# Performance work log

Measured on AMD Instinct MI355X. Metric: run time of the kernel, lower is better.

## Reference

```python
import jax, jax.numpy as jnp
import numpy as np

N_HEADS = 16
D_MODEL = 1024
D_HEAD = 64
B, T = 2, 2048


def setup_inputs() -> dict:
    key = jax.random.key(0)
    k1, k2, k3, k4 = jax.random.split(key, 4)
    query = jax.random.normal(k1, (B, T, D_MODEL), dtype=jnp.float32)
    query_mask = jnp.ones((B, T), dtype=bool)
    attn_prior = jax.random.uniform(k2, (B, T, T), dtype=jnp.float32)
    Wqkv = jax.random.normal(k3, (D_MODEL, 3 * N_HEADS * D_HEAD), dtype=jnp.float32) * (D_MODEL ** -0.5)
    Wo = jax.random.normal(k4, (N_HEADS * D_HEAD, D_MODEL), dtype=jnp.float32) * ((N_HEADS * D_HEAD) ** -0.5)
    return {"query": query, "query_mask": query_mask, "attn_prior": attn_prior, "Wqkv": Wqkv, "Wo": Wo}


def reference(query, query_mask, attn_prior, Wqkv, Wo):
    Bq, Tq, C = query.shape
    H, dh = N_HEADS, D_HEAD
    scale = dh ** -0.5
    qkv = query @ Wqkv  # (B, T, 3*H*dh)
    q, k, v = jnp.split(qkv, 3, axis=-1)
    q = q.reshape(Bq, Tq, H, dh).transpose(0, 2, 1, 3)  # (B, H, T, dh)
    k = k.reshape(Bq, Tq, H, dh).transpose(0, 2, 1, 3)
    v = v.reshape(Bq, Tq, H, dh).transpose(0, 2, 1, 3)

    attn_score = jnp.einsum('bhqd,bhkd->bhqk', q, k) * scale  # (B, H, T, T)

    # padding mask (B,1,T,1)*(B,1,1,T) -> (B,1,T,T)
    pad_mask = query_mask[:, None, :, None] & query_mask[:, None, None, :]
    neg_inf = jnp.float32(-jnp.inf)
    attn_score = jnp.where(pad_mask, attn_score, neg_inf)
    # causal mask
    causal = jnp.tril(jnp.ones((Tq, Tq), dtype=bool))
    attn_score = jnp.where(causal[None, None], attn_score, neg_inf)

    # training-mode log-domain prior mixing (make_prior_window_strict=False)
    eps = jnp.finfo(jnp.float32).tiny
    prior = attn_prior[:, :Tq][:, None] + eps  # (B, 1, T, T)
    attn_score_log = jax.nn.log_softmax(attn_score, axis=-1) + jnp.log(prior)
    attn_prob = jax.nn.softmax(attn_score_log, axis=-1)

    attn_prob = jnp.where(pad_mask, attn_prob, 0.0)
    y = jnp.einsum('bhqk,bhkd->bhqd', attn_prob, v)  # (B, H, T, dh)
    y = y.transpose(0, 2, 1, 3).reshape(Bq, Tq, H * dh)
    out = y @ Wo  # (B, T, d_model)
    return out, attn_prob, attn_score
```

## Files before the change

kernel.cpp:

```cpp
#include <hip/hip_runtime.h>
#include <math.h>

#define T_SEQ 2048
#define NHEADS 16
#define DHEAD 64
#define NB 2
#define DMODEL 1024
#define EPS_TINY 1.17549435e-38f
#define NEG_BIG -3.0e38f

__global__ __launch_bounds__(256) void sgemm_kernel(
    const float* __restrict__ A, const float* __restrict__ B,
    float* __restrict__ C, int M, int N, int K)
{
    __shared__ float As[8][128];
    __shared__ float Bs[8][132];
    const int tid = threadIdx.x;
    const int ty = tid >> 4, tx = tid & 15;
    const int m0 = blockIdx.y * 128, n0 = blockIdx.x * 128;

    const int ar = tid >> 1, ac = (tid & 1) << 2;
    const int br = tid >> 5, bc = (tid & 31) << 2;
    const float* Ap = A + (size_t)(m0 + ar) * K + ac;
    const float* Bp = B + (size_t)br * N + n0 + bc;

    float acc[8][8];
    #pragma unroll
    for (int i = 0; i < 8; ++i)
        #pragma unroll
        for (int j = 0; j < 8; ++j) acc[i][j] = 0.f;

    float4 av = *(const float4*)(Ap);
    float4 bv = *(const float4*)(Bp);

    for (int k0 = 0; k0 < K; k0 += 8) {
        __syncthreads();
        As[ac+0][ar] = av.x; As[ac+1][ar] = av.y;
        As[ac+2][ar] = av.z; As[ac+3][ar] = av.w;
        *(float4*)&Bs[br][bc] = bv;
        __syncthreads();
        if (k0 + 8 < K) {
            av = *(const float4*)(Ap + k0 + 8);
            bv = *(const float4*)(Bp + (size_t)(k0 + 8) * N);
        }
        #pragma unroll
        for (int kk = 0; kk < 8; ++kk) {
            float4 a0 = *(const float4*)&As[kk][ty*8];
            float4 a1 = *(const float4*)&As[kk][ty*8+4];
            float4 b0 = *(const float4*)&Bs[kk][tx*8];
            float4 b1 = *(const float4*)&Bs[kk][tx*8+4];
            float a[8] = {a0.x,a0.y,a0.z,a0.w,a1.x,a1.y,a1.z,a1.w};
            float bb[8] = {b0.x,b0.y,b0.z,b0.w,b1.x,b1.y,b1.z,b1.w};
            #pragma unroll
            for (int i = 0; i < 8; ++i)
                #pragma unroll
                for (int j = 0; j < 8; ++j)
                    acc[i][j] = fmaf(a[i], bb[j], acc[i][j]);
        }
    }
    #pragma unroll
    for (int i = 0; i < 8; ++i) {
        float* crow = C + (size_t)(m0 + ty*8 + i) * N + n0 + tx*8;
        *(float4*)crow     = make_float4(acc[i][0],acc[i][1],acc[i][2],acc[i][3]);
        *(float4*)(crow+4) = make_float4(acc[i][4],acc[i][5],acc[i][6],acc[i][7]);
    }
}

#define SW(r, g) ((((g) ^ ((r) >> 2)) & 15) << 2)

__global__ __launch_bounds__(256) void attn_chunk_kernel(
    const float* __restrict__ qkv, const float* __restrict__ prior,
    float* __restrict__ score, float* __restrict__ party, float* __restrict__ partml)
{
    __shared__ float Qs[64][64];
    __shared__ float KVs[64][64];
    __shared__ float Ps[64][64];

    const int tid = threadIdx.x;
    const int ty = tid >> 4, tx = tid & 15;

    const int f = 79 - (int)blockIdx.x;
    int qt, c;
    if (f < 8)       { qt = f;                      c = 0; }
    else if (f < 24) { qt = 8 + ((f - 8) >> 1);     c = (f - 8) & 1; }
    else if (f < 48) { int g = f - 24; int q3 = g / 3; qt = 16 + q3; c = g - q3*3; }
    else             { int g = f - 48; qt = 24 + (g >> 2); c = g & 3; }
    const int kt0 = c << 3;
    const int kt1 = min(kt0 + 7, qt);

    const int bh = blockIdx.y;
    const int b = bh >> 4, h = bh & 15;
    const int i0 = qt << 6;
    const float scale = 0.125f;

    const float* qbase = qkv + (size_t)b * T_SEQ * (3*DMODEL) + h * DHEAD;
    const float* kbase = qbase + DMODEL;
    float* srow = score + ((size_t)bh * T_SEQ + i0) * T_SEQ;

    #pragma unroll
    for (int u = 0; u < 4; ++u) {
        int idx = tid + (u << 8);
        int r = idx >> 4, g = idx & 15;
        float4 qv = *(const float4*)(qbase + (size_t)(i0 + r) * (3*DMODEL) + (g << 2));
        *(float4*)&Qs[r][SW(r, g)] = qv;
    }

    float m_i[4], l_i[4], y[4][4];
    #pragma unroll
    for (int i = 0; i < 4; ++i) {
        m_i[i] = -INFINITY; l_i[i] = 0.f;
        #pragma unroll
        for (int j = 0; j < 4; ++j) y[i][j] = 0.f;
    }

    for (int kt = kt0; kt <= kt1; ++kt) {
        const int c0 = kt << 6;
        float4 vpre[4];
        __syncthreads();
        #pragma unroll
        for (int u = 0; u < 4; ++u) {
            int idx = tid + (u << 8);
            int r = idx >> 4, g = idx & 15;
            const float* kp = kbase + (size_t)(c0 + r) * (3*DMODEL) + (g << 2);
            float4 kv = *(const float4*)kp;
            vpre[u] = *(const float4*)(kp + DMODEL);
            *(float4*)&KVs[r][SW(r, g)] = kv;
        }
        __syncthreads();

        float acc[4][4];
        #pragma unroll
        for (int i = 0; i < 4; ++i)
            #pragma unroll
            for (int j = 0; j < 4; ++j) acc[i][j] = 0.f;
        #pragma unroll 8
        for (int d4 = 0; d4 < 16; ++d4) {
            float4 a[4], bb[4];
            #pragma unroll
            for (int i = 0; i < 4; ++i)
                a[i] = *(const float4*)&Qs[(ty<<2)+i][SW((ty<<2)+i, d4)];
            #pragma unroll
            for (int j = 0; j < 4; ++j)
                bb[j] = *(const float4*)&KVs[(tx<<2)+j][SW((tx<<2)+j, d4)];
            #pragma unroll
            for (int i = 0; i < 4; ++i)
                #pragma unroll
                for (int j = 0; j < 4; ++j) {
                    acc[i][j] = fmaf(a[i].x, bb[j].x, acc[i][j]);
                    acc[i][j] = fmaf(a[i].y, bb[j].y, acc[i][j]);
                    acc[i][j] = fmaf(a[i].z, bb[j].z, acc[i][j]);
                    acc[i][j] = fmaf(a[i].w, bb[j].w, acc[i][j]);
                }
        }

        #pragma unroll
        for (int i = 0; i < 4; ++i) {
            const int rloc = (ty<<2) + i;
            const int row = i0 + rloc;
            const int cb = c0 + (tx<<2);
            float4 pv = *(const float4*)(prior + ((size_t)b*T_SEQ + row)*T_SEQ + cb);
            float s0 = (cb+0 <= row) ? acc[i][0]*scale : NEG_BIG;
            float s1 = (cb+1 <= row) ? acc[i][1]*scale : NEG_BIG;
            float s2 = (cb+2 <= row) ? acc[i][2]*scale : NEG_BIG;
            float s3 = (cb+3 <= row) ? acc[i][3]*scale : NEG_BIG;
            *(float4*)(srow + (size_t)rloc*T_SEQ + cb) = make_float4(s0,s1,s2,s3);
            float t0 = s0 + logf(pv.x + EPS_TINY);
            float t1 = s1 + logf(pv.y + EPS_TINY);
            float t2 = s2 + logf(pv.z + EPS_TINY);
            float t3 = s3 + logf(pv.w + EPS_TINY);
            float mt = fmaxf(fmaxf(t0,t1), fmaxf(t2,t3));
            #pragma unroll
            for (int off = 1; off < 16; off <<= 1)
                mt = fmaxf(mt, __shfl_xor(mt, off, 64));
            float mn = fmaxf(m_i[i], mt);
            float alpha = expf(m_i[i] - mn);
            float p0 = expf(t0 - mn), p1 = expf(t1 - mn),
                  p2 = expf(t2 - mn), p3 = expf(t3 - mn);
            float ps = p0 + p1 + p2 + p3;
            #pragma unroll
            for (int off = 1; off < 16; off <<= 1)
                ps += __shfl_xor(ps, off, 64);
            l_i[i] = l_i[i]*alpha + ps;
            m_i[i] = mn;
            y[i][0]*=alpha; y[i][1]*=alpha; y[i][2]*=alpha; y[i][3]*=alpha;
            *(float4*)&Ps[rloc][SW(rloc, tx)] = make_float4(p0,p1,p2,p3);
        }
        __syncthreads();
        #pragma unroll
        for (int u = 0; u < 4; ++u) {
            int idx = tid + (u << 8);
            int r = idx >> 4, g = idx & 15;
            *(float4*)&KVs[r][SW(r, g)] = vpre[u];
        }
        __syncthreads();

        #pragma unroll 8
        for (int J = 0; J < 16; ++J) {
            float4 p[4], vv[4];
            #pragma unroll
            for (int i = 0; i < 4; ++i)
                p[i] = *(const float4*)&Ps[(ty<<2)+i][SW((ty<<2)+i, J)];
            #pragma unroll
            for (int m = 0; m < 4; ++m)
                vv[m] = *(const float4*)&KVs[(J<<2)+m][SW((J<<2)+m, tx)];
            #pragma unroll
            for (int i = 0; i < 4; ++i) {
                y[i][0] = fmaf(p[i].x, vv[0].x, y[i][0]);
                y[i][0] = fmaf(p[i].y, vv[1].x, y[i][0]);
                y[i][0] = fmaf(p[i].z, vv[2].x, y[i][0]);
                y[i][0] = fmaf(p[i].w, vv[3].x, y[i][0]);
                y[i][1] = fmaf(p[i].x, vv[0].y, y[i][1]);
                y[i][1] = fmaf(p[i].y, vv[1].y, y[i][1]);
                y[i][1] = fmaf(p[i].z, vv[2].y, y[i][1]);
                y[i][1] = fmaf(p[i].w, vv[3].y, y[i][1]);
                y[i][2] = fmaf(p[i].x, vv[0].z, y[i][2]);
                y[i][2] = fmaf(p[i].y, vv[1].z, y[i][2]);
                y[i][2] = fmaf(p[i].z, vv[2].z, y[i][2]);
                y[i][2] = fmaf(p[i].w, vv[3].z, y[i][2]);
                y[i][3] = fmaf(p[i].x, vv[0].w, y[i][3]);
                y[i][3] = fmaf(p[i].y, vv[1].w, y[i][3]);
                y[i][3] = fmaf(p[i].z, vv[2].w, y[i][3]);
                y[i][3] = fmaf(p[i].w, vv[3].w, y[i][3]);
            }
        }
    }

    float* yp  = party  + ((((size_t)bh*32 + qt)*4 + c) << 12);
    float* mlp = partml + ((((size_t)bh*32 + qt)*4 + c) << 7);
    #pragma unroll
    for (int i = 0; i < 4; ++i) {
        const int rloc = (ty<<2) + i;
        *(float4*)(yp + (rloc<<6) + (tx<<2)) =
            make_float4(y[i][0], y[i][1], y[i][2], y[i][3]);
        if (tx == 0) { mlp[rloc] = m_i[i]; mlp[64 + rloc] = l_i[i]; }
    }
}

__global__ __launch_bounds__(256) void combine_kernel(
    const float* __restrict__ party, const float* __restrict__ partml,
    float* __restrict__ yws, float* __restrict__ Mws)
{
    const int qt = blockIdx.x, bh = blockIdx.y;
    const int b = bh >> 4, h = bh & 15;
    const int t = threadIdx.x;
    const int r = t >> 2, q = t & 3;
    const int C = (qt >> 3) + 1;
    const size_t base = ((size_t)bh*32 + qt) << 2;

    float m[4], l[4];
    float M = -INFINITY;
    for (int cc = 0; cc < C; ++cc) {
        m[cc] = partml[((base + cc) << 7) + r];
        l[cc] = partml[((base + cc) << 7) + 64 + r];
        M = fmaxf(M, m[cc]);
    }
    float w[4];
    float L = 0.f;
    for (int cc = 0; cc < C; ++cc) { w[cc] = expf(m[cc] - M); L += l[cc] * w[cc]; }
    const float invL = 1.0f / L;

    float* yp = yws + ((size_t)b*T_SEQ + (qt<<6) + r)*DMODEL + h*DHEAD;
    #pragma unroll
    for (int d4 = 0; d4 < 4; ++d4) {
        const int d = (q << 4) + (d4 << 2);
        float4 acc = make_float4(0.f, 0.f, 0.f, 0.f);
        for (int cc = 0; cc < C; ++cc) {
            float4 v = *(const float4*)(party + ((base + cc) << 12) + (r << 6) + d);
            acc.x = fmaf(w[cc], v.x, acc.x);
            acc.y = fmaf(w[cc], v.y, acc.y);
            acc.z = fmaf(w[cc], v.z, acc.z);
            acc.w = fmaf(w[cc], v.w, acc.w);
        }
        *(float4*)(yp + d) = make_float4(acc.x*invL, acc.y*invL, acc.z*invL, acc.w*invL);
    }
    if (q == 0) Mws[(size_t)bh*T_SEQ + (qt<<6) + r] = M + logf(L);
}

__global__ __launch_bounds__(256) void prob_kernel(
    const float* __restrict__ score, const float* __restrict__ prior,
    const float* __restrict__ Mws, float* __restrict__ prob,
    float* __restrict__ score_w)
{
    const size_t e = ((size_t)blockIdx.x * 256 + threadIdx.x) << 2;
    const int j  = (int)(e & (size_t)(T_SEQ - 1));
    const int i  = (int)((e >> 11) & (size_t)(T_SEQ - 1));
    if (j > i) {
        *(float4*)(score_w + e) = make_float4(NEG_BIG, NEG_BIG, NEG_BIG, NEG_BIG);
        *(float4*)(prob + e)    = make_float4(0.f, 0.f, 0.f, 0.f);
        return;
    }
    const int bh = (int)(e >> 22);
    const int b  = bh >> 4;
    const float M = Mws[((size_t)bh << 11) + i];
    float4 s = *(const float4*)(score + e);
    float4 p = *(const float4*)(prior + ((((size_t)b << 11) + i) << 11) + j);
    float4 o;
    o.x = expf(s.x + logf(p.x + EPS_TINY) - M);
    o.y = expf(s.y + logf(p.y + EPS_TINY) - M);
    o.z = expf(s.z + logf(p.z + EPS_TINY) - M);
    o.w = expf(s.w + logf(p.w + EPS_TINY) - M);
    *(float4*)(prob + e) = o;
}

extern "C" void kernel_launch(void* const* d_in, const int* in_sizes, int n_in,
                              void* d_out, int out_size, void* d_ws, size_t ws_size,
                              hipStream_t stream) {
    const float* query = (const float*)d_in[0];
    const float* prior = (const float*)d_in[2];
    const float* Wqkv  = (const float*)d_in[3];
    const float* Wo    = (const float*)d_in[4];

    float* out   = (float*)d_out;
    float* prob  = out  + (size_t)NB*T_SEQ*DMODEL;
    float* score = prob + (size_t)NB*NHEADS*T_SEQ*T_SEQ;

    float* qkv_ws = (float*)d_ws;
    float* y_ws   = qkv_ws + (size_t)NB*T_SEQ*3*DMODEL;
    float* M_ws   = y_ws   + (size_t)NB*T_SEQ*DMODEL;

    float* party  = prob;
    float* partml = prob + ((size_t)32*32*4*4096);

    sgemm_kernel<<<dim3((3*DMODEL)/128, (NB*T_SEQ)/128), 256, 0, stream>>>(
        query, Wqkv, qkv_ws, NB*T_SEQ, 3*DMODEL, DMODEL);
    attn_chunk_kernel<<<dim3(80, NB*NHEADS), 256, 0, stream>>>(
        qkv_ws, prior, score, party, partml);
    combine_kernel<<<dim3(T_SEQ/64, NB*NHEADS), 256, 0, stream>>>(
        party, partml, y_ws, M_ws);
    prob_kernel<<<dim3((unsigned)((size_t)NB*NHEADS*T_SEQ*T_SEQ/4/256)), 256, 0, stream>>>(
        score, prior, M_ws, prob, score);
    sgemm_kernel<<<dim3(DMODEL/128, (NB*T_SEQ)/128), 256, 0, stream>>>(
        y_ws, Wo, out, NB*T_SEQ, DMODEL, DMODEL);
}
```

Measured before the change: 1.964 ms.

## Replace FP32 SIMT GEMMs with split-bf16 triple MFMA GEMMs

Both projection GEMMs move from a scalar FP32 register-tiled kernel to an MFMA kernel. Each operand is split into high and low bf16 parts and three products are accumulated, which approximates FP32 accuracy. New cast kernels split and transpose the inputs and weights into scratch space inside the prob output buffer. The output projection now runs before prob_kernel, so it must finish before prob overwrites that scratch. The cast passes add extra memory traffic and launches, but the GEMMs are a small part of the runtime next to the T×T attention kernels.

```diff
diff --git a/kernel.cpp b/kernel.cpp
--- a/kernel.cpp
+++ b/kernel.cpp
@@ -9,60 +9,153 @@
 #define EPS_TINY 1.17549435e-38f
 #define NEG_BIG -3.0e38f
 
-__global__ __launch_bounds__(256) void sgemm_kernel(
-    const float* __restrict__ A, const float* __restrict__ B,
+typedef __attribute__((ext_vector_type(8))) short bf16x8;
+typedef __attribute__((ext_vector_type(4))) float f32x4;
+
+__device__ __forceinline__ ushort rne_bf16(float x) {
+    unsigned u = __float_as_uint(x);
+    return (ushort)((u + 0x7FFFu + ((u >> 16) & 1u)) >> 16);
+}
+
+__global__ __launch_bounds__(256) void cast_split(
+    const float* __restrict__ x, ushort* __restrict__ hi, ushort* __restrict__ lo,
+    int n4)
+{
+    int i = blockIdx.x * 256 + threadIdx.x;
+    if (i >= n4) return;
+    float4 v = *(const float4*)(x + 4 * (size_t)i);
+    float vv[4] = {v.x, v.y, v.z, v.w};
+    ushort h[4], l[4];
+    #pragma unroll
+    for (int j = 0; j < 4; ++j) {
+        h[j] = rne_bf16(vv[j]);
+        float hf = __uint_as_float((unsigned)h[j] << 16);
+        l[j] = rne_bf16(vv[j] - hf);
+    }
+    *(ushort4*)(hi + 4 * (size_t)i) = make_ushort4(h[0], h[1], h[2], h[3]);
+    *(ushort4*)(lo + 4 * (size_t)i) = make_ushort4(l[0], l[1], l[2], l[3]);
+}
+
+__global__ __launch_bounds__(256) void cast_splitT(
+    const float* __restrict__ in, ushort* __restrict__ thi, ushort* __restrict__ tlo,
+    int K, int N)
+{
+    __shared__ float tile[64][65];
+    const int k0 = blockIdx.y * 64, n0 = blockIdx.x * 64;
+    const int t = threadIdx.x;
+    const int r = t >> 4, c4 = (t & 15) << 2;
+    #pragma unroll
+    for (int u = 0; u < 4; ++u) {
+        int row = r + u * 16;
+        float4 v = *(const float4*)(in + (size_t)(k0 + row) * N + n0 + c4);
+        tile[row][c4+0] = v.x; tile[row][c4+1] = v.y;
+        tile[row][c4+2] = v.z; tile[row][c4+3] = v.w;
+    }
+    __syncthreads();
+    const int n = t >> 2, ks = (t & 3) << 4;
+    ushort hb[16], lb[16];
+    #pragma unroll
+    for (int j = 0; j < 16; ++j) {
+        float xv = tile[ks + j][n];
+        ushort h = rne_bf16(xv);
+        hb[j] = h;
+        lb[j] = rne_bf16(xv - __uint_as_float((unsigned)h << 16));
+    }
+    ushort* ph = thi + (size_t)(n0 + n) * K + k0 + ks;
+    ushort* pl = tlo + (size_t)(n0 + n) * K + k0 + ks;
+    #pragma unroll
+    for (int j = 0; j < 16; j += 4) {
+        *(ushort4*)(ph + j) = make_ushort4(hb[j], hb[j+1], hb[j+2], hb[j+3]);
+        *(ushort4*)(pl + j) = make_ushort4(lb[j], lb[j+1], lb[j+2], lb[j+3]);
+    }
+}
+
+__global__ __launch_bounds__(256) void gemm_bf16x3(
+    const ushort* __restrict__ Ahi, const ushort* __restrict__ Alo,
+    const ushort* __restrict__ Bthi, const ushort* __restrict__ Btlo,
     float* __restrict__ C, int M, int N, int K)
 {
-    __shared__ float As[8][128];
-    __shared__ float Bs[8][132];
+    __shared__ ushort Ah[128*32], Al[128*32], Bh[128*32], Bl[128*32];
     const int tid = threadIdx.x;
-    const int ty = tid >> 4, tx = tid & 15;
+    const int wid = tid >> 6, lane = tid & 63;
+    const int wr = wid >> 1, wc = wid & 1;
     const int m0 = blockIdx.y * 128, n0 = blockIdx.x * 128;
 
-    const int ar = tid >> 1, ac = (tid & 1) << 2;
-    const int br = tid >> 5, bc = (tid & 31) << 2;
-    const float* Ap = A + (size_t)(m0 + ar) * K + ac;
-    const float* Bp = B + (size_t)br * N + n0 + bc;
-
-    float acc[8][8];
-    #pragma unroll
-    for (int i = 0; i < 8; ++i)
-        #pragma unroll
-        for (int j = 0; j < 8; ++j) acc[i][j] = 0.f;
-
-    float4 av = *(const float4*)(Ap);
-    float4 bv = *(const float4*)(Bp);
-
-    for (int k0 = 0; k0 < K; k0 += 8) {
-        __syncthreads();
-        As[ac+0][ar] = av.x; As[ac+1][ar] = av.y;
-        As[ac+2][ar] = av.z; As[ac+3][ar] = av.w;
-        *(float4*)&Bs[br][bc] = bv;
-        __syncthreads();
-        if (k0 + 8 < K) {
-            av = *(const float4*)(Ap + k0 + 8);
-            bv = *(const float4*)(Bp + (size_t)(k0 + 8) * N);
-        }
-        #pragma unroll
-        for (int kk = 0; kk < 8; ++kk) {
-            float4 a0 = *(const float4*)&As[kk][ty*8];
-            float4 a1 = *(const float4*)&As[kk][ty*8+4];
-            float4 b0 = *(const float4*)&Bs[kk][tx*8];
-            float4 b1 = *(const float4*)&Bs[kk][tx*8+4];
-            float a[8] = {a0.x,a0.y,a0.z,a0.w,a1.x,a1.y,a1.z,a1.w};
-            float bb[8] = {b0.x,b0.y,b0.z,b0.w,b1.x,b1.y,b1.z,b1.w};
-            #pragma unroll
-            for (int i = 0; i < 8; ++i)
-                #pragma unroll
-                for (int j = 0; j < 8; ++j)
-                    acc[i][j] = fmaf(a[i], bb[j], acc[i][j]);
-        }
-    }
-    #pragma unroll
-    for (int i = 0; i < 8; ++i) {
-        float* crow = C + (size_t)(m0 + ty*8 + i) * N + n0 + tx*8;
-        *(float4*)crow     = make_float4(acc[i][0],acc[i][1],acc[i][2],acc[i][3]);
-        *(float4*)(crow+4) = make_float4(acc[i][4],acc[i][5],acc[i][6],acc[i][7]);
+    const int sr = tid >> 1;
+    const int ss = (tid & 1) << 4;
+    const int q0 = (tid & 1) << 1;
+    const int sw0 = sr * 32 + ((q0    ) ^ (sr & 3)) * 8;
+    const int sw1 = sr * 32 + ((q0 + 1) ^ (sr & 3)) * 8;
+
+    const ushort* apH = Ahi  + (size_t)(m0 + sr) * K + ss;
+    const ushort* apL = Alo  + (size_t)(m0 + sr) * K + ss;
+    const ushort* bpH = Bthi + (size_t)(n0 + sr) * K + ss;
+    const ushort* bpL = Btlo + (size_t)(n0 + sr) * K + ss;
+
+    f32x4 acc[4][4];
+    #pragma unroll
+    for (int i = 0; i < 4; ++i)
+        #pragma unroll
+        for (int j = 0; j < 4; ++j) acc[i][j] = (f32x4){0.f, 0.f, 0.f, 0.f};
+
+    uint4 pAh0 = *(const uint4*)(apH),     pAh1 = *(const uint4*)(apH + 8);
+    uint4 pAl0 = *(const uint4*)(apL),     pAl1 = *(const uint4*)(apL + 8);
+    uint4 pBh0 = *(const uint4*)(bpH),     pBh1 = *(const uint4*)(bpH + 8);
+    uint4 pBl0 = *(const uint4*)(bpL),     pBl1 = *(const uint4*)(bpL + 8);
+
+    int offA[4], offB[4];
+    #pragma unroll
+    for (int f = 0; f < 4; ++f) {
+        int ra = wr * 64 + f * 16 + (lane & 15);
+        int rb = wc * 64 + f * 16 + (lane & 15);
+        offA[f] = ra * 32 + (((lane >> 4) ^ (ra & 3)) * 8);
+        offB[f] = rb * 32 + (((lane >> 4) ^ (rb & 3)) * 8);
+    }
+
+    for (int k0 = 0; k0 < K; k0 += 32) {
+        __syncthreads();
+        *(uint4*)&Ah[sw0] = pAh0;  *(uint4*)&Ah[sw1] = pAh1;
+        *(uint4*)&Al[sw0] = pAl0;  *(uint4*)&Al[sw1] = pAl1;
+        *(uint4*)&Bh[sw0] = pBh0;  *(uint4*)&Bh[sw1] = pBh1;
+        *(uint4*)&Bl[sw0] = pBl0;  *(uint4*)&Bl[sw1] = pBl1;
+        __syncthreads();
+        if (k0 + 32 < K) {
+            pAh0 = *(const uint4*)(apH + k0 + 32);  pAh1 = *(const uint4*)(apH + k0 + 40);
+            pAl0 = *(const uint4*)(apL + k0 + 32);  pAl1 = *(const uint4*)(apL + k0 + 40);
+            pBh0 = *(const uint4*)(bpH + k0 + 32);  pBh1 = *(const uint4*)(bpH + k0 + 40);
+            pBl0 = *(const uint4*)(bpL + k0 + 32);  pBl1 = *(const uint4*)(bpL + k0 + 40);
+        }
+        bf16x8 ah[4], al[4], bh[4], bl[4];
+        #pragma unroll
+        for (int f = 0; f < 4; ++f) {
+            ah[f] = *(const bf16x8*)&Ah[offA[f]];
+            al[f] = *(const bf16x8*)&Al[offA[f]];
+            bh[f] = *(const bf16x8*)&Bh[offB[f]];
+            bl[f] = *(const bf16x8*)&Bl[offB[f]];
+        }
+        #pragma unroll
+        for (int fm = 0; fm < 4; ++fm)
+            #pragma unroll
+            for (int fn = 0; fn < 4; ++fn) {
+                acc[fm][fn] = __builtin_amdgcn_mfma_f32_16x16x32_bf16(
+                    ah[fm], bh[fn], acc[fm][fn], 0, 0, 0);
+                acc[fm][fn] = __builtin_amdgcn_mfma_f32_16x16x32_bf16(
+                    ah[fm], bl[fn], acc[fm][fn], 0, 0, 0);
+                acc[fm][fn] = __builtin_amdgcn_mfma_f32_16x16x32_bf16(
+                    al[fm], bh[fn], acc[fm][fn], 0, 0, 0);
+            }
+    }
+
+    #pragma unroll
+    for (int fm = 0; fm < 4; ++fm) {
+        const int row = m0 + wr * 64 + fm * 16 + ((lane >> 4) << 2);
+        #pragma unroll
+        for (int fn = 0; fn < 4; ++fn) {
+            const int col = n0 + wc * 64 + fn * 16 + (lane & 15);
+            #pragma unroll
+            for (int r = 0; r < 4; ++r)
+                C[(size_t)(row + r) * N + col] = acc[fm][fn][r];
+        }
     }
 }
 
@@ -320,15 +413,31 @@
 
     float* party  = prob;
     float* partml = prob + ((size_t)32*32*4*4096);
-
-    sgemm_kernel<<<dim3((3*DMODEL)/128, (NB*T_SEQ)/128), 256, 0, stream>>>(
-        query, Wqkv, qkv_ws, NB*T_SEQ, 3*DMODEL, DMODEL);
+    ushort* SC = (ushort*)(prob + (size_t)24*1024*1024);
+    const size_t Mi = 1024*1024;
+    ushort* A1hi = SC;              ushort* A1lo = SC + 4*Mi;
+    ushort* B1hi = SC + 8*Mi;       ushort* B1lo = SC + 11*Mi;
+    ushort* B2hi = SC + 14*Mi;      ushort* B2lo = SC + 15*Mi;
+    ushort* Yhi  = SC + 16*Mi;      ushort* Ylo  = SC + 20*Mi;
+
+    const int M1 = NB*T_SEQ;
+
+    cast_split<<<dim3(M1*DMODEL/4/256), 256, 0, stream>>>(query, A1hi, A1lo, M1*DMODEL/4);
+    cast_splitT<<<dim3(3*DMODEL/64, DMODEL/64), 256, 0, stream>>>(Wqkv, B1hi, B1lo, DMODEL, 3*DMODEL);
+    cast_splitT<<<dim3(DMODEL/64, DMODEL/64), 256, 0, stream>>>(Wo, B2hi, B2lo, DMODEL, DMODEL);
+
+    gemm_bf16x3<<<dim3(3*DMODEL/128, M1/128), 256, 0, stream>>>(
+        A1hi, A1lo, B1hi, B1lo, qkv_ws, M1, 3*DMODEL, DMODEL);
+
     attn_chunk_kernel<<<dim3(80, NB*NHEADS), 256, 0, stream>>>(
         qkv_ws, prior, score, party, partml);
     combine_kernel<<<dim3(T_SEQ/64, NB*NHEADS), 256, 0, stream>>>(
         party, partml, y_ws, M_ws);
+
+    cast_split<<<dim3(M1*DMODEL/4/256), 256, 0, stream>>>(y_ws, Yhi, Ylo, M1*DMODEL/4);
+    gemm_bf16x3<<<dim3(DMODEL/128, M1/128), 256, 0, stream>>>(
+        Yhi, Ylo, B2hi, B2lo, out, M1, DMODEL, DMODEL);
+
     prob_kernel<<<dim3((unsigned)((size_t)NB*NHEADS*T_SEQ*T_SEQ/4/256)), 256, 0, stream>>>(
         score, prior, M_ws, prob, score);
-    sgemm_kernel<<<dim3(DMODEL/128, (NB*T_SEQ)/128), 256, 0, stream>>>(
-        y_ws, Wo, out, NB*T_SEQ, DMODEL, DMODEL);
-}
+}
```

Result: faster. 1.675 ms (-14.7%).
